# Optimization experiments

Measured on AMD Instinct MI355X. Metric: run time of the kernel, lower is better.

Reference implementation:

```python
import jax, jax.numpy as jnp
import numpy as np

# dims per init_kwargs / input_specs
B, S, HID = 4, 2048, 1024
H = 16          # num_heads
DH = HID // H   # head_dim = 64
G = 1024        # group_size; grouped feature dim = S*DH//G = 128
SCALE = 1.0 / (DH ** 0.5)


def setup_inputs() -> dict:
    key = jax.random.key(0)
    ks = jax.random.split(key, 9)
    w = lambda k: jax.random.normal(k, (HID, HID), jnp.float32) * 0.02
    b = lambda k: jax.random.normal(k, (HID,), jnp.float32) * 0.02
    return {
        "hidden_states": jax.random.normal(ks[0], (B, S, HID), jnp.float32),
        "Wq": w(ks[1]), "bq": b(ks[2]),
        "Wk": w(ks[3]), "bk": b(ks[4]),
        "Wv": w(ks[5]), "bv": b(ks[6]),
        "Wo": w(ks[7]), "bo": b(ks[8]),
    }


def reference(hidden_states, Wq, bq, Wk, bk, Wv, bv, Wo, bo):
    Bs, Ss, _ = hidden_states.shape

    def proj(W, bias):
        # torch nn.Linear: x @ W.T + b
        y = hidden_states @ W.T + bias                      # [B,S,HID]
        y = y.reshape(Bs, Ss, H, DH).transpose(0, 2, 1, 3)  # [B,H,S,DH]
        # grouped view: fold seq/head_dim into G groups of S*DH//G features
        return y.reshape(Bs, H, G, -1)                      # [B,H,G,S*DH/G]

    q, k, v = proj(Wq, bq), proj(Wk, bk), proj(Wv, bv)
    scores = jnp.einsum("bhgd,bhkd->bhgk", q, k) * SCALE    # [B,H,G,G]
    probs = jax.nn.softmax(scores, axis=-1)                 # dropout: eval mode (identity)
    ctx = jnp.einsum("bhgk,bhkd->bhgd", probs, v)           # [B,H,G,S*DH/G]
    ctx = ctx.transpose(0, 2, 1, 3).reshape(Bs, -1, HID)    # [B,S,HID]
    return ctx @ Wo.T + bo
```

## Files before the change

kernel.cpp:

```cpp
#include <hip/hip_runtime.h>


typedef __attribute__((ext_vector_type(8))) short short8;
typedef __attribute__((ext_vector_type(4))) float f32x4;
typedef unsigned int u32;
typedef unsigned short u16;

#define MFMA16(a, b, c) __builtin_amdgcn_mfma_f32_16x16x32_bf16((a), (b), (c), 0, 0, 0)

union S8 { short8 s; uint2 v[2]; u32 u[4]; };

__device__ __forceinline__ u32 f2bf1(float x) {
    union { float f; u32 u; } v; v.f = x;
    return (v.u + 0x7fffu + ((v.u >> 16) & 1u)) >> 16;
}

__device__ __forceinline__ u32 cvtpk(float lo, float hi) {
    u32 r;
    asm("v_cvt_pk_bf16_f32 %0, %1, %2" : "=v"(r) : "v"(lo), "v"(hi));
    return r;
}

__device__ __forceinline__ void gld16(u16* lds, const u16* g) {
    __builtin_amdgcn_global_load_lds(
        (const __attribute__((address_space(1))) unsigned int*)(g),
        (__attribute__((address_space(3))) unsigned int*)(lds),
        16, 0, 0);
}

__global__ __launch_bounds__(256) void convert(
    const float* __restrict__ X, const float* __restrict__ Wq,
    const float* __restrict__ Wk, const float* __restrict__ Wv,
    const float* __restrict__ Wo,
    u16* __restrict__ Xb, u16* __restrict__ Wcat, u16* __restrict__ Wob)
{
    const size_t M8 = 8388608, M1 = 1048576;
    size_t i = ((size_t)blockIdx.x * 256 + threadIdx.x) * 16;
    const float* src; u16* dst;
    if (i < M8)              { src = X  + i;                dst = Xb   + i; }
    else if (i < M8 + M1)    { src = Wq + (i - M8);         dst = Wcat + (i - M8); }
    else if (i < M8 + 2*M1)  { src = Wk + (i - M8 - M1);    dst = Wcat + (i - M8); }
    else if (i < M8 + 3*M1)  { src = Wv + (i - M8 - 2*M1);  dst = Wcat + (i - M8); }
    else                     { src = Wo + (i - M8 - 3*M1);  dst = Wob  + (i - M8 - 3*M1); }
#pragma unroll
    for (int j = 0; j < 2; ++j) {
        float4 a = ((const float4*)src)[2 * j];
        float4 b = ((const float4*)src)[2 * j + 1];
        uint4 o;
        o.x = f2bf1(a.x) | (f2bf1(a.y) << 16);
        o.y = f2bf1(a.z) | (f2bf1(a.w) << 16);
        o.z = f2bf1(b.x) | (f2bf1(b.y) << 16);
        o.w = f2bf1(b.z) | (f2bf1(b.w) << 16);
        ((uint4*)dst)[j] = o;
    }
}

__global__ __launch_bounds__(256, 3) void qkv_gemm9(
    const u16* __restrict__ Xb, const u16* __restrict__ Wcat,
    const float* __restrict__ b0, const float* __restrict__ b1,
    const float* __restrict__ b2,
    u16* __restrict__ q_att, u16* __restrict__ k_att, u16* __restrict__ v_t)
{
    const int nb = blockIdx.x, mb = blockIdx.y;
    const int mat = nb >> 3;

    __shared__ __align__(16) u16 As[128 * 64];
    __shared__ __align__(16) u16 Bs[128 * 64];

    const int t = threadIdx.x, wave = t >> 6, lane = t & 63;
    const int l15 = lane & 15, quad = lane >> 4;
    const int wm = (wave >> 1) * 64, wn = (wave & 1) * 64;

    const int srow = t >> 3;
    const int scol = ((t & 7) ^ (srow & 7)) * 8;
    u16* ldsA = As + wave * 512;
    u16* ldsB = Bs + wave * 512;

    const u16* Ab = Xb   + (size_t)(mb * 128) * 1024;
    const u16* Bb = Wcat + (size_t)(nb * 128) * 1024;

    const int swz = l15 & 7;

    f32x4 acc[4][4] = {};

    for (int k0 = 0; k0 < 1024; k0 += 64) {
        __syncthreads();
#pragma unroll
        for (int c = 0; c < 4; ++c) {
            size_t so = (size_t)(c * 32 + srow) * 1024 + k0 + scol;
            gld16(ldsA + c * 2048, Ab + so);
            gld16(ldsB + c * 2048, Bb + so);
        }
        __syncthreads();

#pragma unroll
        for (int ks = 0; ks < 2; ++ks) {
            short8 af[4], bf[4];
            const int ck = ((ks * 4 + quad) ^ swz) * 8;
#pragma unroll
            for (int mt = 0; mt < 4; ++mt)
                af[mt] = *(const short8*)(As + (wm + mt * 16 + l15) * 64 + ck);
#pragma unroll
            for (int nt = 0; nt < 4; ++nt)
                bf[nt] = *(const short8*)(Bs + (wn + nt * 16 + l15) * 64 + ck);
#pragma unroll
            for (int mt = 0; mt < 4; ++mt)
#pragma unroll
                for (int nt = 0; nt < 4; ++nt)
                    acc[mt][nt] = MFMA16(af[mt], bf[nt], acc[mt][nt]);
        }
    }

    const float* bias = (mat == 0) ? b0 : (mat == 1) ? b1 : b2;
    const float scl = (mat == 0) ? 0.125f : 1.0f;
#pragma unroll
    for (int nt = 0; nt < 4; ++nt) {
        int colm = (nb & 7) * 128 + wn + nt * 16 + l15;
        float bv = bias[colm];
        int h = colm >> 6, dh = colm & 63;
#pragma unroll
        for (int mt = 0; mt < 4; ++mt) {
            int row0 = mb * 128 + wm + mt * 16 + quad * 4;
            int b = row0 >> 11, s0 = row0 & 2047;
            int bh = b * 16 + h, g0 = s0 >> 1;
            float v0 = (acc[mt][nt][0] + bv) * scl, v1 = (acc[mt][nt][1] + bv) * scl;
            float v2 = (acc[mt][nt][2] + bv) * scl, v3 = (acc[mt][nt][3] + bv) * scl;
            if (mat == 2) {
                u32 w0 = f2bf1(v0) | (f2bf1(v2) << 16);
                u32 w1 = f2bf1(v1) | (f2bf1(v3) << 16);
                int j6 = g0 & 63;
                int gp = (g0 & ~63) + (j6 & 32) + ((j6 >> 2) & 3) * 8
                       + ((j6 >> 4) & 1) * 4 + (j6 & 3);
                *(u32*)(v_t + ((size_t)(bh * 128 + dh) * 1024 + gp)) = w0;
                *(u32*)(v_t + ((size_t)(bh * 128 + dh + 64) * 1024 + gp)) = w1;
            } else {
                u16* dst = (mat == 0) ? q_att : k_att;
                u32 w0 = f2bf1(v0) | (f2bf1(v1) << 16);
                u32 w1 = f2bf1(v2) | (f2bf1(v3) << 16);
                size_t base = ((size_t)bh * 1024 + g0) * 128 + 2 * dh;
                *(u32*)(dst + base) = w0;
                *(u32*)(dst + base + 128) = w1;
            }
        }
    }
}

__global__ __launch_bounds__(256, 2) void attn5(
    const u16* __restrict__ q_att, const u16* __restrict__ k_att,
    const u16* __restrict__ v_t, u16* __restrict__ ctx)
{
    const int bh = blockIdx.x, qb = blockIdx.y;
    const u16* Q = q_att + (size_t)bh * 131072;
    const u16* K = k_att + (size_t)bh * 131072;
    const u16* V = v_t  + (size_t)bh * 131072;

    __shared__ __align__(16) u16 Ks[2][64 * 128];
    __shared__ __align__(16) u16 Vs[2][128 * 64];

    const int t = threadIdx.x, wave = t >> 6, lane = t & 63;
    const int l15 = lane & 15, quad = lane >> 4;

    int offK[4], offV[4];
#pragma unroll
    for (int j = 0; j < 4; ++j) {
        int ck = wave * 4 + j;
        int rowK = ck * 4 + (lane >> 4);
        offK[j] = rowK * 128 + (((lane & 15) ^ (rowK & 15)) * 8);
        int rowV = ck * 8 + (lane >> 3);
        offV[j] = rowV * 1024 + (((lane & 7) ^ ((lane >> 3) & 7)) * 8);
    }

#define ASTAGE(pp, kt) do {                                                   \
        const u16* Kt_ = K + (size_t)(kt) * 8192;                             \
        const u16* Vt_ = V + (size_t)(kt) * 64;                               \
        _Pragma("unroll")                                                     \
        for (int j_ = 0; j_ < 4; ++j_) {                                      \
            gld16(&Ks[(pp)][(wave * 4 + j_) * 512], Kt_ + offK[j_]);          \
            gld16(&Vs[(pp)][(wave * 4 + j_) * 512], Vt_ + offV[j_]);          \
        }                                                                     \
    } while (0)

    short8 bq[2][4];
#pragma unroll
    for (int qg = 0; qg < 2; ++qg) {
        const int qr = qb * 128 + wave * 32 + qg * 16 + l15;
#pragma unroll
        for (int kb = 0; kb < 4; ++kb)
            bq[qg][kb] = *(const short8*)(Q + (size_t)qr * 128 + kb * 32 + quad * 8);
    }

    f32x4 accO[2][8] = {};
    float m_i[2] = {-1e30f, -1e30f}, l_i[2] = {0.0f, 0.0f};

    ASTAGE(0, 0);
    __syncthreads();

    for (int kt = 0; kt < 16; ++kt) {
        const int p = kt & 1;
        if (kt + 1 < 16) ASTAGE(p ^ 1, kt + 1);
        const u16* Ksp = &Ks[p][0];
        const u16* Vsp = &Vs[p][0];

        f32x4 accS[2][4] = {};
        __builtin_amdgcn_s_setprio(1);
#pragma unroll
        for (int kf = 0; kf < 4; ++kf)
#pragma unroll
            for (int kb = 0; kb < 4; ++kb) {
                short8 ak = *(const short8*)(Ksp + (kf * 16 + l15) * 128
                                             + (((kb * 4 + quad) ^ l15) * 8));
                accS[0][kf] = MFMA16(ak, bq[0][kb], accS[0][kf]);
                accS[1][kf] = MFMA16(ak, bq[1][kb], accS[1][kf]);
            }
        __builtin_amdgcn_s_setprio(0);

        u32 pb[2][8];
#pragma unroll
        for (int qg = 0; qg < 2; ++qg) {
            float mloc = -1e30f;
#pragma unroll
            for (int kf = 0; kf < 4; ++kf)
                mloc = fmaxf(mloc, fmaxf(fmaxf(accS[qg][kf][0], accS[qg][kf][1]),
                                         fmaxf(accS[qg][kf][2], accS[qg][kf][3])));
            mloc = fmaxf(mloc, __shfl_xor(mloc, 16));
            mloc = fmaxf(mloc, __shfl_xor(mloc, 32));

            if (!__all(mloc - m_i[qg] <= 8.0f)) {
                float mn = fmaxf(m_i[qg], mloc);
                float alpha = __expf(m_i[qg] - mn);
#pragma unroll
                for (int f = 0; f < 8; ++f) {
                    accO[qg][f][0] *= alpha; accO[qg][f][1] *= alpha;
                    accO[qg][f][2] *= alpha; accO[qg][f][3] *= alpha;
                }
                l_i[qg] *= alpha;
                m_i[qg] = mn;
            }

            float lsum = 0.0f;
            const float mi = m_i[qg];
#pragma unroll
            for (int kf = 0; kf < 4; ++kf) {
                float p0 = __expf(accS[qg][kf][0] - mi);
                float p1 = __expf(accS[qg][kf][1] - mi);
                float p2 = __expf(accS[qg][kf][2] - mi);
                float p3 = __expf(accS[qg][kf][3] - mi);
                lsum += (p0 + p1) + (p2 + p3);
                pb[qg][kf * 2]     = cvtpk(p0, p1);
                pb[qg][kf * 2 + 1] = cvtpk(p2, p3);
            }
            lsum += __shfl_xor(lsum, 16);
            lsum += __shfl_xor(lsum, 32);
            l_i[qg] += lsum;
        }

        S8 bp00, bp01, bp10, bp11;
        bp00.u[0] = pb[0][0]; bp00.u[1] = pb[0][1]; bp00.u[2] = pb[0][2]; bp00.u[3] = pb[0][3];
        bp01.u[0] = pb[0][4]; bp01.u[1] = pb[0][5]; bp01.u[2] = pb[0][6]; bp01.u[3] = pb[0][7];
        bp10.u[0] = pb[1][0]; bp10.u[1] = pb[1][1]; bp10.u[2] = pb[1][2]; bp10.u[3] = pb[1][3];
        bp11.u[0] = pb[1][4]; bp11.u[1] = pb[1][5]; bp11.u[2] = pb[1][6]; bp11.u[3] = pb[1][7];
        const int l7 = l15 & 7;
        __builtin_amdgcn_s_setprio(1);
#pragma unroll
        for (int df = 0; df < 8; ++df) {
            const u16* vrow = Vsp + (df * 16 + l15) * 64;
            short8 av0 = *(const short8*)(vrow + ((quad ^ l7) * 8));
            short8 av1 = *(const short8*)(vrow + (((quad + 4) ^ l7) * 8));
            accO[0][df] = MFMA16(av0, bp00.s, accO[0][df]);
            accO[0][df] = MFMA16(av1, bp01.s, accO[0][df]);
            accO[1][df] = MFMA16(av0, bp10.s, accO[1][df]);
            accO[1][df] = MFMA16(av1, bp11.s, accO[1][df]);
        }
        __builtin_amdgcn_s_setprio(0);

        if (kt + 1 < 16) __syncthreads();
    }
#undef ASTAGE

    const int h = bh & 15, b = bh >> 4;
#pragma unroll
    for (int qg = 0; qg < 2; ++qg) {
        const int qr = qb * 128 + wave * 32 + qg * 16 + l15;
        float inv = 1.0f / l_i[qg];
        size_t base = ((size_t)(b * 2048 + 2 * qr + (h >> 3))) * 1024 + (h & 7) * 128;
#pragma unroll
        for (int df = 0; df < 8; ++df) {
            int dp = df * 16 + quad * 4;
            uint2 w;
            w.x = f2bf1(accO[qg][df][0] * inv) | (f2bf1(accO[qg][df][1] * inv) << 16);
            w.y = f2bf1(accO[qg][df][2] * inv) | (f2bf1(accO[qg][df][3] * inv) << 16);
            *(uint2*)(ctx + base + dp) = w;
        }
    }
}

__global__ __launch_bounds__(256, 3) void out_gemm9(
    const u16* __restrict__ ctx, const u16* __restrict__ Wob,
    const float* __restrict__ bo, float* __restrict__ out)
{
    const int nb = blockIdx.x, mb = blockIdx.y;
    __shared__ __align__(16) u16 As[128 * 64];
    __shared__ __align__(16) u16 Bs[128 * 64];
    const int t = threadIdx.x, wave = t >> 6, lane = t & 63;
    const int l15 = lane & 15, quad = lane >> 4;
    const int wm = (wave >> 1) * 64, wn = (wave & 1) * 64;

    const int srow = t >> 3;
    const int scol = ((t & 7) ^ (srow & 7)) * 8;
    u16* ldsA = As + wave * 512;
    u16* ldsB = Bs + wave * 512;

    const u16* Ab = ctx + (size_t)(mb * 128) * 1024;
    const u16* Bb = Wob + (size_t)(nb * 128) * 1024;

    const int swz = l15 & 7;

    f32x4 acc[4][4] = {};

    for (int k0 = 0; k0 < 1024; k0 += 64) {
        __syncthreads();
#pragma unroll
        for (int c = 0; c < 4; ++c) {
            size_t so = (size_t)(c * 32 + srow) * 1024 + k0 + scol;
            gld16(ldsA + c * 2048, Ab + so);
            gld16(ldsB + c * 2048, Bb + so);
        }
        __syncthreads();

#pragma unroll
        for (int ks = 0; ks < 2; ++ks) {
            short8 af[4], bf[4];
            const int ck = ((ks * 4 + quad) ^ swz) * 8;
#pragma unroll
            for (int mt = 0; mt < 4; ++mt)
                af[mt] = *(const short8*)(As + (wm + mt * 16 + l15) * 64 + ck);
#pragma unroll
            for (int nt = 0; nt < 4; ++nt)
                bf[nt] = *(const short8*)(Bs + (wn + nt * 16 + l15) * 64 + ck);
#pragma unroll
            for (int mt = 0; mt < 4; ++mt)
#pragma unroll
                for (int nt = 0; nt < 4; ++nt)
                    acc[mt][nt] = MFMA16(af[mt], bf[nt], acc[mt][nt]);
        }
    }

#pragma unroll
    for (int nt = 0; nt < 4; ++nt) {
        int col = nb * 128 + wn + nt * 16 + l15;
        float bv = bo[col];
#pragma unroll
        for (int mt = 0; mt < 4; ++mt)
#pragma unroll
            for (int r = 0; r < 4; ++r) {
                int row = mb * 128 + wm + mt * 16 + quad * 4 + r;
                out[(size_t)row * 1024 + col] = acc[mt][nt][r] + bv;
            }
    }
}

extern "C" void kernel_launch(void* const* d_in, const int* in_sizes, int n_in,
                              void* d_out, int out_size, void* d_ws, size_t ws_size,
                              hipStream_t stream)
{
    const float* X  = (const float*)d_in[0];
    const float* Wq = (const float*)d_in[1];
    const float* bq = (const float*)d_in[2];
    const float* Wk = (const float*)d_in[3];
    const float* bk = (const float*)d_in[4];
    const float* Wv = (const float*)d_in[5];
    const float* bv = (const float*)d_in[6];
    const float* Wo = (const float*)d_in[7];
    const float* bo = (const float*)d_in[8];

    const size_t M8 = 8388608;
    u16* q_att = (u16*)d_ws;
    u16* k_att = q_att + M8;
    u16* v_t   = k_att + M8;
    u16* Xb    = v_t   + M8;
    u16* ctx   = Xb;
    u16* Wcat  = Xb + M8;
    u16* Wob   = Wcat + 3 * 1048576;

    convert<<<dim3(3072), 256, 0, stream>>>(X, Wq, Wk, Wv, Wo, Xb, Wcat, Wob);
    qkv_gemm9<<<dim3(24, 64), 256, 0, stream>>>(Xb, Wcat, bq, bk, bv,
                                                q_att, k_att, v_t);
    attn5<<<dim3(64, 8), 256, 0, stream>>>(q_att, k_att, v_t, ctx);
    out_gemm9<<<dim3(8, 64), 256, 0, stream>>>(ctx, Wob, bo, (float*)d_out);
}
```

Before: 238.1 us.

## Double-buffer LDS tiles in QKV and output GEMMs to overlap loads with MFMA

New measurement: 242.0 us. Within noise of the previous version (+1.6%).

```diff
diff --git a/kernel.cpp b/kernel.cpp
--- a/kernel.cpp
+++ b/kernel.cpp
@@ -55,7 +55,7 @@
     }
 }
 
-__global__ __launch_bounds__(256, 3) void qkv_gemm9(
+__global__ __launch_bounds__(256, 2) void qkv_gemm10(
     const u16* __restrict__ Xb, const u16* __restrict__ Wcat,
     const float* __restrict__ b0, const float* __restrict__ b1,
     const float* __restrict__ b2,
@@ -64,8 +64,8 @@
     const int nb = blockIdx.x, mb = blockIdx.y;
     const int mat = nb >> 3;
 
-    __shared__ __align__(16) u16 As[128 * 64];
-    __shared__ __align__(16) u16 Bs[128 * 64];
+    __shared__ __align__(16) u16 As[2][128 * 64];
+    __shared__ __align__(16) u16 Bs[2][128 * 64];
 
     const int t = threadIdx.x, wave = t >> 6, lane = t & 63;
     const int l15 = lane & 15, quad = lane >> 4;
@@ -73,25 +73,31 @@
 
     const int srow = t >> 3;
     const int scol = ((t & 7) ^ (srow & 7)) * 8;
-    u16* ldsA = As + wave * 512;
-    u16* ldsB = Bs + wave * 512;
 
     const u16* Ab = Xb   + (size_t)(mb * 128) * 1024;
     const u16* Bb = Wcat + (size_t)(nb * 128) * 1024;
 
     const int swz = l15 & 7;
 
+#define QSTAGE(pp, k0_) do {                                                  \
+        _Pragma("unroll")                                                     \
+        for (int c_ = 0; c_ < 4; ++c_) {                                      \
+            size_t so_ = (size_t)(c_ * 32 + srow) * 1024 + (k0_) + scol;      \
+            gld16(&As[(pp)][wave * 512 + c_ * 2048], Ab + so_);               \
+            gld16(&Bs[(pp)][wave * 512 + c_ * 2048], Bb + so_);               \
+        }                                                                     \
+    } while (0)
+
     f32x4 acc[4][4] = {};
 
-    for (int k0 = 0; k0 < 1024; k0 += 64) {
-        __syncthreads();
-#pragma unroll
-        for (int c = 0; c < 4; ++c) {
-            size_t so = (size_t)(c * 32 + srow) * 1024 + k0 + scol;
-            gld16(ldsA + c * 2048, Ab + so);
-            gld16(ldsB + c * 2048, Bb + so);
-        }
-        __syncthreads();
+    QSTAGE(0, 0);
+    __syncthreads();
+
+    for (int kt = 0; kt < 16; ++kt) {
+        const int p = kt & 1;
+        if (kt + 1 < 16) QSTAGE(p ^ 1, (kt + 1) * 64);
+        const u16* Asp = &As[p][0];
+        const u16* Bsp = &Bs[p][0];
 
 #pragma unroll
         for (int ks = 0; ks < 2; ++ks) {
@@ -99,17 +105,20 @@
             const int ck = ((ks * 4 + quad) ^ swz) * 8;
 #pragma unroll
             for (int mt = 0; mt < 4; ++mt)
-                af[mt] = *(const short8*)(As + (wm + mt * 16 + l15) * 64 + ck);
+                af[mt] = *(const short8*)(Asp + (wm + mt * 16 + l15) * 64 + ck);
 #pragma unroll
             for (int nt = 0; nt < 4; ++nt)
-                bf[nt] = *(const short8*)(Bs + (wn + nt * 16 + l15) * 64 + ck);
+                bf[nt] = *(const short8*)(Bsp + (wn + nt * 16 + l15) * 64 + ck);
 #pragma unroll
             for (int mt = 0; mt < 4; ++mt)
 #pragma unroll
                 for (int nt = 0; nt < 4; ++nt)
                     acc[mt][nt] = MFMA16(af[mt], bf[nt], acc[mt][nt]);
         }
-    }
+
+        if (kt + 1 < 16) __syncthreads();
+    }
+#undef QSTAGE
 
     const float* bias = (mat == 0) ? b0 : (mat == 1) ? b1 : b2;
     const float scl = (mat == 0) ? 0.125f : 1.0f;
@@ -294,38 +303,44 @@
     }
 }
 
-__global__ __launch_bounds__(256, 3) void out_gemm9(
+__global__ __launch_bounds__(256, 2) void out_gemm10(
     const u16* __restrict__ ctx, const u16* __restrict__ Wob,
     const float* __restrict__ bo, float* __restrict__ out)
 {
     const int nb = blockIdx.x, mb = blockIdx.y;
-    __shared__ __align__(16) u16 As[128 * 64];
-    __shared__ __align__(16) u16 Bs[128 * 64];
+    __shared__ __align__(16) u16 As[2][128 * 64];
+    __shared__ __align__(16) u16 Bs[2][128 * 64];
     const int t = threadIdx.x, wave = t >> 6, lane = t & 63;
     const int l15 = lane & 15, quad = lane >> 4;
     const int wm = (wave >> 1) * 64, wn = (wave & 1) * 64;
 
     const int srow = t >> 3;
     const int scol = ((t & 7) ^ (srow & 7)) * 8;
-    u16* ldsA = As + wave * 512;
-    u16* ldsB = Bs + wave * 512;
 
     const u16* Ab = ctx + (size_t)(mb * 128) * 1024;
     const u16* Bb = Wob + (size_t)(nb * 128) * 1024;
 
     const int swz = l15 & 7;
 
+#define OSTAGE(pp, k0_) do {                                                  \
+        _Pragma("unroll")                                                     \
+        for (int c_ = 0; c_ < 4; ++c_) {                                      \
+            size_t so_ = (size_t)(c_ * 32 + srow) * 1024 + (k0_) + scol;      \
+            gld16(&As[(pp)][wave * 512 + c_ * 2048], Ab + so_);               \
+            gld16(&Bs[(pp)][wave * 512 + c_ * 2048], Bb + so_);               \
+        }                                                                     \
+    } while (0)
+
     f32x4 acc[4][4] = {};
 
-    for (int k0 = 0; k0 < 1024; k0 += 64) {
-        __syncthreads();
-#pragma unroll
-        for (int c = 0; c < 4; ++c) {
-            size_t so = (size_t)(c * 32 + srow) * 1024 + k0 + scol;
-            gld16(ldsA + c * 2048, Ab + so);
-            gld16(ldsB + c * 2048, Bb + so);
-        }
-        __syncthreads();
+    OSTAGE(0, 0);
+    __syncthreads();
+
+    for (int kt = 0; kt < 16; ++kt) {
+        const int p = kt & 1;
+        if (kt + 1 < 16) OSTAGE(p ^ 1, (kt + 1) * 64);
+        const u16* Asp = &As[p][0];
+        const u16* Bsp = &Bs[p][0];
 
 #pragma unroll
         for (int ks = 0; ks < 2; ++ks) {
@@ -333,17 +348,20 @@
             const int ck = ((ks * 4 + quad) ^ swz) * 8;
 #pragma unroll
             for (int mt = 0; mt < 4; ++mt)
-                af[mt] = *(const short8*)(As + (wm + mt * 16 + l15) * 64 + ck);
+                af[mt] = *(const short8*)(Asp + (wm + mt * 16 + l15) * 64 + ck);
 #pragma unroll
             for (int nt = 0; nt < 4; ++nt)
-                bf[nt] = *(const short8*)(Bs + (wn + nt * 16 + l15) * 64 + ck);
+                bf[nt] = *(const short8*)(Bsp + (wn + nt * 16 + l15) * 64 + ck);
 #pragma unroll
             for (int mt = 0; mt < 4; ++mt)
 #pragma unroll
                 for (int nt = 0; nt < 4; ++nt)
                     acc[mt][nt] = MFMA16(af[mt], bf[nt], acc[mt][nt]);
         }
-    }
+
+        if (kt + 1 < 16) __syncthreads();
+    }
+#undef OSTAGE
 
 #pragma unroll
     for (int nt = 0; nt < 4; ++nt) {
@@ -383,8 +401,8 @@
     u16* Wob   = Wcat + 3 * 1048576;
 
     convert<<<dim3(3072), 256, 0, stream>>>(X, Wq, Wk, Wv, Wo, Xb, Wcat, Wob);
-    qkv_gemm9<<<dim3(24, 64), 256, 0, stream>>>(Xb, Wcat, bq, bk, bv,
-                                                q_att, k_att, v_t);
+    qkv_gemm10<<<dim3(24, 64), 256, 0, stream>>>(Xb, Wcat, bq, bk, bv,
+                                                 q_att, k_att, v_t);
     attn5<<<dim3(64, 8), 256, 0, stream>>>(q_att, k_att, v_t, ctx);
-    out_gemm9<<<dim3(8, 64), 256, 0, stream>>>(ctx, Wob, bo, (float*)d_out);
-}
+    out_gemm10<<<dim3(8, 64), 256, 0, stream>>>(ctx, Wob, bo, (float*)d_out);
+}
```
